# Optimization experiments

Measured on AMD Instinct MI355X. Metric: run time of the kernel, lower is better.

The kernel has to match this reference:

```python
import jax, jax.numpy as jnp
import numpy as np

FP8_MAX = 448.0  # torch.finfo(torch.float8_e4m3fn).max

def per_tensor_quantize(t):
    amax = jnp.max(jnp.abs(t))
    scale = FP8_MAX / jnp.maximum(amax, 1e-12)
    q = jnp.clip(t * scale, -FP8_MAX, FP8_MAX).astype(jnp.float8_e4m3fn)
    return q, (1.0 / scale).astype(jnp.float32)

def fp8_gemm(q, a_scale, w_q, w_scale, out_dtype):
    # emulate: linear(A.to(out)*a_scale, B.to(out)*b_scale)
    A = q.astype(out_dtype) * a_scale
    B = w_q.astype(out_dtype) * w_scale
    return A @ B.T

def setup_inputs() -> dict:
    key = jax.random.key(0)
    k1, k2, k3, k4 = jax.random.split(key, 4)
    tokens, hidden, ffn = 4096, 4096, 10752
    return {
        "x": jax.random.normal(k1, (tokens, hidden), jnp.float32),
        "expert_w1": jax.random.normal(k2, (ffn, hidden), jnp.float32) * 0.02,
        "expert_v1": jax.random.normal(k3, (ffn, hidden), jnp.float32) * 0.02,
        "expert_w2": jax.random.normal(k4, (ffn, hidden), jnp.float32) * 0.02,
    }

def reference(x, expert_w1, expert_v1, expert_w2):
    dt = x.dtype
    # weight quantization (as done in _quantize_weights per expert)
    w1_q, w1_s = per_tensor_quantize(expert_w1)
    v1_q, v1_s = per_tensor_quantize(expert_v1)
    w2_q, w2_s = per_tensor_quantize(expert_w2)
    # activation quantization + gate/up GEMMs
    qin, x_s = per_tensor_quantize(x)
    gate = fp8_gemm(qin, x_s, w1_q, w1_s, dt)          # [N, ffn]
    up = fp8_gemm(qin, x_s, v1_q, v1_s, dt)            # [N, ffn]
    inter = jax.nn.silu(gate) * up                      # fused GLU
    qmid, m_s = per_tensor_quantize(inter)
    # down proj uses expert_w2.t() -> B = [hidden, ffn]
    down = fp8_gemm(qmid, m_s, w2_q.T, w2_s, dt)        # [N, hidden]
    return down
```

## Files before the change

kernel.cpp:

```cpp
#include <hip/hip_runtime.h>
#include <cstdint>
#include <cstddef>

typedef float f32x4 __attribute__((ext_vector_type(4)));
typedef float f32x16 __attribute__((ext_vector_type(16)));
typedef int i32x4 __attribute__((ext_vector_type(4)));
typedef int i32x8 __attribute__((ext_vector_type(8)));
typedef unsigned char u8;

static __device__ __forceinline__ void gload_lds16(const void* g, void* l) {
  __builtin_amdgcn_global_load_lds(
      (__attribute__((address_space(1))) void*)(void*)g,
      (__attribute__((address_space(3))) void*)l,
      16, 0, 0);
}

#if defined(__has_builtin)
#if __has_builtin(__builtin_amdgcn_cvt_pk_fp8_f32)
#define HAVE_HW_FP8 1
#endif
#endif

__device__ __forceinline__ u8 f32_to_e4m3_sw(float x) {
  unsigned s = (__float_as_uint(x) >> 24) & 0x80;
  float ax = fabsf(x);
  if (!(ax > 0.0f)) return (u8)s;
  if (ax >= 448.0f) return (u8)(s | 0x7e);
  if (ax < 0.015625f) {
    int m = (int)rintf(ax * 512.0f);
    if (m >= 8) return (u8)(s | 0x08);
    return (u8)(s | m);
  }
  int e = ilogbf(ax);
  int m = (int)rintf(ldexpf(ax, 3 - e));
  if (m == 16) { ++e; m = 8; }
  return (u8)(s | ((e + 7) << 3) | (m - 8));
}

__device__ __forceinline__ unsigned cvt4_fp8(float a, float b, float c, float d) {
#ifdef HAVE_HW_FP8
  int lo = __builtin_amdgcn_cvt_pk_fp8_f32(a, b, 0, false);
  return (unsigned)__builtin_amdgcn_cvt_pk_fp8_f32(c, d, lo, true);
#else
  return (unsigned)f32_to_e4m3_sw(a) | ((unsigned)f32_to_e4m3_sw(b) << 8) |
         ((unsigned)f32_to_e4m3_sw(c) << 16) | ((unsigned)f32_to_e4m3_sw(d) << 24);
#endif
}

__global__ __launch_bounds__(256) void amax_kernel(const float* __restrict__ src, size_t n4,
                                                   unsigned* __restrict__ out) {
  float m = 0.0f;
  size_t stride = (size_t)gridDim.x * blockDim.x;
  const f32x4* p = (const f32x4*)src;
  for (size_t i = (size_t)blockIdx.x * blockDim.x + threadIdx.x; i < n4; i += stride) {
    f32x4 v = p[i];
    m = fmaxf(m, fmaxf(fmaxf(fabsf(v[0]), fabsf(v[1])), fmaxf(fabsf(v[2]), fabsf(v[3]))));
  }
#pragma unroll
  for (int off = 32; off > 0; off >>= 1) m = fmaxf(m, __shfl_down(m, off));
  __shared__ float red[4];
  int lane = threadIdx.x & 63, wid = threadIdx.x >> 6;
  if (lane == 0) red[wid] = m;
  __syncthreads();
  if (threadIdx.x == 0) {
    float v = fmaxf(fmaxf(red[0], red[1]), fmaxf(red[2], red[3]));
    atomicMax(out, __float_as_uint(v));
  }
}

__global__ __launch_bounds__(256) void quant_kernel(const float* __restrict__ src,
                                                    u8* __restrict__ dst,
                                                    const unsigned* __restrict__ amax_bits,
                                                    size_t n8) {
  float amax = __uint_as_float(*amax_bits);
  float scale = 448.0f / fmaxf(amax, 1e-12f);
  size_t stride = (size_t)gridDim.x * blockDim.x;
  const f32x4* p = (const f32x4*)src;
  uint2* q = (uint2*)dst;
  for (size_t i = (size_t)blockIdx.x * blockDim.x + threadIdx.x; i < n8; i += stride) {
    f32x4 a = p[2 * i], b = p[2 * i + 1];
    float a0 = fminf(fmaxf(a[0] * scale, -448.f), 448.f);
    float a1 = fminf(fmaxf(a[1] * scale, -448.f), 448.f);
    float a2 = fminf(fmaxf(a[2] * scale, -448.f), 448.f);
    float a3 = fminf(fmaxf(a[3] * scale, -448.f), 448.f);
    float b0 = fminf(fmaxf(b[0] * scale, -448.f), 448.f);
    float b1 = fminf(fmaxf(b[1] * scale, -448.f), 448.f);
    float b2 = fminf(fmaxf(b[2] * scale, -448.f), 448.f);
    float b3 = fminf(fmaxf(b[3] * scale, -448.f), 448.f);
    uint2 r;
    r.x = cvt4_fp8(a0, a1, a2, a3);
    r.y = cvt4_fp8(b0, b1, b2, b3);
    q[i] = r;
  }
}

__global__ __launch_bounds__(256) void quantT_kernel(const float* __restrict__ src,
                                                     u8* __restrict__ dst,
                                                     const unsigned* __restrict__ amax_bits,
                                                     int R, int C) {
  __shared__ float t[64][65];
  float amax = __uint_as_float(*amax_bits);
  float scale = 448.0f / fmaxf(amax, 1e-12f);
  int nbr = R >> 6;
  int br = (int)blockIdx.x % nbr, bc = (int)blockIdx.x / nbr;
  int r0 = br * 64, c0 = bc * 64;
  int tid = threadIdx.x;
  int lc = tid & 63, lr = tid >> 6;
#pragma unroll
  for (int i = 0; i < 16; ++i)
    t[lr + i * 4][lc] = src[(size_t)(r0 + lr + i * 4) * C + c0 + lc];
  __syncthreads();
  int qd = tid & 15, xbase = tid >> 4;
#pragma unroll
  for (int i = 0; i < 4; ++i) {
    int x = xbase + 16 * i;
    float v0 = fminf(fmaxf(t[4 * qd + 0][x] * scale, -448.f), 448.f);
    float v1 = fminf(fmaxf(t[4 * qd + 1][x] * scale, -448.f), 448.f);
    float v2 = fminf(fmaxf(t[4 * qd + 2][x] * scale, -448.f), 448.f);
    float v3 = fminf(fmaxf(t[4 * qd + 3][x] * scale, -448.f), 448.f);
    *(unsigned*)(dst + (size_t)(c0 + x) * R + r0 + 4 * qd) = cvt4_fp8(v0, v1, v2, v3);
  }
}

__device__ __forceinline__ int swz_key(int r) { return (r >> 2) & 3; }

__device__ __forceinline__ int swz_off32(int r, int h) {
  return r * 64 + ((((h << 1) ^ swz_key(r)) << 4));
}

__device__ __forceinline__ i32x8 ld_frag(const u8* base, int r, int h) {
  int o = swz_off32(r, h);
  i32x8 f;
  f.lo = *(const i32x4*)(base + o);
  f.hi = *(const i32x4*)(base + (o ^ 16));
  return f;
}

#define MFMA_MX(a, b, c) \
  __builtin_amdgcn_mfma_scale_f32_32x32x64_f8f6f4((a), (b), (c), 0, 0, 0, 0x7F7F7F7F, 0, 0x7F7F7F7F)

__global__ __launch_bounds__(512, 4) void gemm1_gateup(
    const u8* __restrict__ Aq, const u8* __restrict__ Wq, const u8* __restrict__ Vq,
    const unsigned* __restrict__ scal, float* __restrict__ inter,
    unsigned* __restrict__ amax_mid, int M, int N, int K) {
  __shared__ __align__(16) u8 lA[8192], lW[8192], lV[8192];
  __shared__ float red[8];
  int tid = threadIdx.x;
  int lane = tid & 63, wid = tid >> 6;
  int wm = wid >> 2, wn = wid & 3;

  int nbn = N >> 7;
  int nwg = (int)gridDim.x;
  int bid = (int)blockIdx.x;
  int cpx = nwg >> 3;
  int swz = (bid & 7) * cpx + (bid >> 3);
  int bm = swz / nbn, bn = swz - bm * nbn;

  int r0 = tid >> 2;
  int kblk = ((tid & 3) ^ swz_key(r0)) << 4;
  const u8* aS = Aq + (size_t)(bm * 128 + r0) * K + kblk;
  const u8* wS = Wq + (size_t)(bn * 128 + r0) * K + kblk;
  const u8* vS = Vq + (size_t)(bn * 128 + r0) * K + kblk;

  f32x16 g0 = (f32x16)(0.f), g1 = (f32x16)(0.f);
  f32x16 u0 = (f32x16)(0.f), u1 = (f32x16)(0.f);

  int rfrag = lane & 31;
  int h = lane >> 5;
  int arow = wm * 64 + rfrag;
  int wrow = wn * 32 + rfrag;

  for (int kt = 0; kt < K; kt += 64) {
    __syncthreads();
    gload_lds16(aS + kt, lA + tid * 16);
    gload_lds16(wS + kt, lW + tid * 16);
    gload_lds16(vS + kt, lV + tid * 16);
    __syncthreads();
    i32x8 a0 = ld_frag(lA, arow, h);
    i32x8 a1 = ld_frag(lA, arow + 32, h);
    i32x8 w0 = ld_frag(lW, wrow, h);
    i32x8 v0 = ld_frag(lV, wrow, h);
    g0 = MFMA_MX(a0, w0, g0);
    g1 = MFMA_MX(a1, w0, g1);
    u0 = MFMA_MX(a0, v0, u0);
    u1 = MFMA_MX(a1, v0, u1);
  }

  float ax = __uint_as_float(scal[0]);
  float aw = __uint_as_float(scal[1]);
  float av = __uint_as_float(scal[2]);
  float inv_x = 1.0f / (448.0f / fmaxf(ax, 1e-12f));
  float inv_w = 1.0f / (448.0f / fmaxf(aw, 1e-12f));
  float inv_v = 1.0f / (448.0f / fmaxf(av, 1e-12f));
  float sg = inv_x * inv_w, su = inv_x * inv_v;

  int rb = bm * 128 + wm * 64 + h * 4;
  int cb = bn * 128 + wn * 32 + rfrag;
  float lmax = 0.0f;
#pragma unroll
  for (int mi = 0; mi < 2; ++mi) {
    const f32x16& gg = mi ? g1 : g0;
    const f32x16& uu = mi ? u1 : u0;
#pragma unroll
    for (int q = 0; q < 16; ++q) {
      int rr = rb + mi * 32 + (q & 3) + 8 * (q >> 2);
      float gv = gg[q] * sg;
      float uv = uu[q] * su;
      float iv = gv / (1.0f + expf(-gv)) * uv;
      inter[(size_t)rr * N + cb] = iv;
      lmax = fmaxf(lmax, fabsf(iv));
    }
  }
#pragma unroll
  for (int off = 32; off > 0; off >>= 1) lmax = fmaxf(lmax, __shfl_down(lmax, off));
  if (lane == 0) red[wid] = lmax;
  __syncthreads();
  if (tid == 0) {
    float v = red[0];
#pragma unroll
    for (int i = 1; i < 8; ++i) v = fmaxf(v, red[i]);
    atomicMax(amax_mid, __float_as_uint(v));
  }
}

__global__ __launch_bounds__(512, 4) void gemm2_down(
    const u8* __restrict__ Aq, const u8* __restrict__ Bq,
    const unsigned* __restrict__ amax_a, const unsigned* __restrict__ amax_b,
    float* __restrict__ out, int M, int N, int K) {
  __shared__ __align__(16) u8 lA[8192], lB[16384];
  int tid = threadIdx.x;
  int lane = tid & 63, wid = tid >> 6;
  int wm = wid >> 2, wn = wid & 3;

  int nbn = N >> 8;
  int nwg = (int)gridDim.x;
  int bid = (int)blockIdx.x;
  int cpx = nwg >> 3;
  int swz = (bid & 7) * cpx + (bid >> 3);
  int bm = swz / nbn, bn = swz - bm * nbn;

  int r0 = tid >> 2;
  int kblk = ((tid & 3) ^ swz_key(r0)) << 4;
  const u8* aS = Aq + (size_t)(bm * 128 + r0) * K + kblk;
  const u8* bS = Bq + (size_t)(bn * 256 + r0) * K + kblk;
  size_t rK = (size_t)128 * K;

  f32x16 c00 = (f32x16)(0.f), c01 = (f32x16)(0.f);
  f32x16 c10 = (f32x16)(0.f), c11 = (f32x16)(0.f);

  int rfrag = lane & 31;
  int h = lane >> 5;
  int arow = wm * 64 + rfrag;
  int brow = wn * 64 + rfrag;

  for (int kt = 0; kt < K; kt += 64) {
    __syncthreads();
    gload_lds16(aS + kt, lA + tid * 16);
    gload_lds16(bS + kt, lB + tid * 16);
    gload_lds16(bS + kt + rK, lB + 8192 + tid * 16);
    __syncthreads();
    i32x8 a0 = ld_frag(lA, arow, h);
    i32x8 a1 = ld_frag(lA, arow + 32, h);
    i32x8 b0 = ld_frag(lB, brow, h);
    i32x8 b1 = ld_frag(lB, brow + 32, h);
    c00 = MFMA_MX(a0, b0, c00);
    c01 = MFMA_MX(a0, b1, c01);
    c10 = MFMA_MX(a1, b0, c10);
    c11 = MFMA_MX(a1, b1, c11);
  }

  float sa = 1.0f / (448.0f / fmaxf(__uint_as_float(*amax_a), 1e-12f));
  float sb = 1.0f / (448.0f / fmaxf(__uint_as_float(*amax_b), 1e-12f));
  float sc = sa * sb;

  int rb = bm * 128 + wm * 64 + h * 4;
  int cb = bn * 256 + wn * 64 + rfrag;
#pragma unroll
  for (int mi = 0; mi < 2; ++mi)
#pragma unroll
    for (int ni = 0; ni < 2; ++ni) {
      const f32x16& cc = mi ? (ni ? c11 : c10) : (ni ? c01 : c00);
#pragma unroll
      for (int q = 0; q < 16; ++q) {
        int rr = rb + mi * 32 + (q & 3) + 8 * (q >> 2);
        out[(size_t)rr * N + (cb + ni * 32)] = cc[q] * sc;
      }
    }
}

extern "C" void kernel_launch(void* const* d_in, const int* in_sizes, int n_in,
                              void* d_out, int out_size, void* d_ws, size_t ws_size,
                              hipStream_t stream) {
  const float* x  = (const float*)d_in[0];
  const float* w1 = (const float*)d_in[1];
  const float* v1 = (const float*)d_in[2];
  const float* w2 = (const float*)d_in[3];
  const int M = 4096, H = 4096, F = 10752;

  u8* ws = (u8*)d_ws;
  unsigned* scal = (unsigned*)ws;
  u8* xq   = ws + 256;
  u8* w1q  = xq   + (size_t)M * H;
  u8* v1q  = w1q  + (size_t)F * H;
  u8* w2qT = v1q  + (size_t)F * H;
  u8* midq = w2qT + (size_t)F * H;
  float* inter = (float*)(midq + (size_t)M * F);

  hipMemsetAsync(scal, 0, 256, stream);
  amax_kernel<<<2048, 256, 0, stream>>>(x,  (size_t)M * H / 4, scal + 0);
  amax_kernel<<<2048, 256, 0, stream>>>(w1, (size_t)F * H / 4, scal + 1);
  amax_kernel<<<2048, 256, 0, stream>>>(v1, (size_t)F * H / 4, scal + 2);
  amax_kernel<<<2048, 256, 0, stream>>>(w2, (size_t)F * H / 4, scal + 3);

  quant_kernel<<<2048, 256, 0, stream>>>(x,  xq,  scal + 0, (size_t)M * H / 8);
  quant_kernel<<<2048, 256, 0, stream>>>(w1, w1q, scal + 1, (size_t)F * H / 8);
  quant_kernel<<<2048, 256, 0, stream>>>(v1, v1q, scal + 2, (size_t)F * H / 8);
  quantT_kernel<<<(F / 64) * (H / 64), 256, 0, stream>>>(w2, w2qT, scal + 3, F, H);

  gemm1_gateup<<<(M / 128) * (F / 128), 512, 0, stream>>>(xq, w1q, v1q, scal, inter,
                                                          scal + 4, M, F, H);
  quant_kernel<<<2048, 256, 0, stream>>>(inter, midq, scal + 4, (size_t)M * F / 8);
  gemm2_down<<<(M / 128) * (H / 256), 512, 0, stream>>>(midq, w2qT, scal + 4, scal + 3,
                                                        (float*)d_out, M, H, F);
}
```

Measured before the change: 1.018 ms.

## Triple-buffer LDS with async prefetch and 4-wave tiles in both FP8 GEMMs

Both GEMM kernels move from 8-wave blocks with a load/sync/compute loop to 4-wave blocks that each compute a 64x64 sub-tile. K-tiles go into a 3-stage LDS ring, with prefetches issued two tiles ahead, explicit vmcnt waits, barriers and MFMA priority bumps, so global-to-LDS loads overlap the MFMA work. gemm2 shrinks its N tile from 256 to 128, which doubles its grid. In exchange, LDS use per block rises and each wave holds more accumulator registers, which may reduce occupancy.

```diff
diff --git a/kernel.cpp b/kernel.cpp
--- a/kernel.cpp
+++ b/kernel.cpp
@@ -139,15 +139,15 @@
 #define MFMA_MX(a, b, c) \
   __builtin_amdgcn_mfma_scale_f32_32x32x64_f8f6f4((a), (b), (c), 0, 0, 0, 0x7F7F7F7F, 0, 0x7F7F7F7F)
 
-__global__ __launch_bounds__(512, 4) void gemm1_gateup(
+__global__ __launch_bounds__(256, 2) void gemm1_gateup(
     const u8* __restrict__ Aq, const u8* __restrict__ Wq, const u8* __restrict__ Vq,
     const unsigned* __restrict__ scal, float* __restrict__ inter,
     unsigned* __restrict__ amax_mid, int M, int N, int K) {
-  __shared__ __align__(16) u8 lA[8192], lW[8192], lV[8192];
-  __shared__ float red[8];
+  __shared__ __align__(16) u8 lA[3][8192], lW[3][8192], lV[3][8192];
+  __shared__ float red[4];
   int tid = threadIdx.x;
   int lane = tid & 63, wid = tid >> 6;
-  int wm = wid >> 2, wn = wid & 3;
+  int wm = wid >> 1, wn = wid & 1;
 
   int nbn = N >> 7;
   int nwg = (int)gridDim.x;
@@ -161,29 +161,74 @@
   const u8* aS = Aq + (size_t)(bm * 128 + r0) * K + kblk;
   const u8* wS = Wq + (size_t)(bn * 128 + r0) * K + kblk;
   const u8* vS = Vq + (size_t)(bn * 128 + r0) * K + kblk;
-
-  f32x16 g0 = (f32x16)(0.f), g1 = (f32x16)(0.f);
-  f32x16 u0 = (f32x16)(0.f), u1 = (f32x16)(0.f);
+  size_t rK = (size_t)64 * K;
+
+  f32x16 g00 = (f32x16)(0.f), g01 = (f32x16)(0.f), g10 = (f32x16)(0.f), g11 = (f32x16)(0.f);
+  f32x16 u00 = (f32x16)(0.f), u01 = (f32x16)(0.f), u10 = (f32x16)(0.f), u11 = (f32x16)(0.f);
 
   int rfrag = lane & 31;
   int h = lane >> 5;
   int arow = wm * 64 + rfrag;
-  int wrow = wn * 32 + rfrag;
-
-  for (int kt = 0; kt < K; kt += 64) {
-    __syncthreads();
-    gload_lds16(aS + kt, lA + tid * 16);
-    gload_lds16(wS + kt, lW + tid * 16);
-    gload_lds16(vS + kt, lV + tid * 16);
-    __syncthreads();
-    i32x8 a0 = ld_frag(lA, arow, h);
-    i32x8 a1 = ld_frag(lA, arow + 32, h);
-    i32x8 w0 = ld_frag(lW, wrow, h);
-    i32x8 v0 = ld_frag(lV, wrow, h);
-    g0 = MFMA_MX(a0, w0, g0);
-    g1 = MFMA_MX(a1, w0, g1);
-    u0 = MFMA_MX(a0, v0, u0);
-    u1 = MFMA_MX(a1, v0, u1);
+  int brow = wn * 64 + rfrag;
+
+  int NT = K >> 6;
+  {
+    gload_lds16(aS + 0, lA[0] + tid * 16);
+    gload_lds16(aS + 0 + rK, lA[0] + 4096 + tid * 16);
+    gload_lds16(wS + 0, lW[0] + tid * 16);
+    gload_lds16(wS + 0 + rK, lW[0] + 4096 + tid * 16);
+    gload_lds16(vS + 0, lV[0] + tid * 16);
+    gload_lds16(vS + 0 + rK, lV[0] + 4096 + tid * 16);
+    gload_lds16(aS + 64, lA[1] + tid * 16);
+    gload_lds16(aS + 64 + rK, lA[1] + 4096 + tid * 16);
+    gload_lds16(wS + 64, lW[1] + tid * 16);
+    gload_lds16(wS + 64 + rK, lW[1] + 4096 + tid * 16);
+    gload_lds16(vS + 64, lV[1] + tid * 16);
+    gload_lds16(vS + 64 + rK, lV[1] + 4096 + tid * 16);
+  }
+
+  for (int t = 0; t < NT; ++t) {
+    int cur = t % 3;
+    int nx = cur + 2; if (nx >= 3) nx -= 3;
+    int kt2 = (t + 2) * 64;
+    bool do_stage = (t + 2) < NT;
+    if (t + 1 < NT) {
+      asm volatile("s_waitcnt vmcnt(6)" ::: "memory");
+    } else {
+      asm volatile("s_waitcnt vmcnt(0)" ::: "memory");
+    }
+    __builtin_amdgcn_s_barrier();
+    i32x8 a0 = ld_frag(lA[cur], arow, h);
+    i32x8 a1 = ld_frag(lA[cur], arow + 32, h);
+    i32x8 w0 = ld_frag(lW[cur], brow, h);
+    i32x8 w1 = ld_frag(lW[cur], brow + 32, h);
+    if (do_stage) {
+      gload_lds16(aS + kt2, lA[nx] + tid * 16);
+      gload_lds16(aS + kt2 + rK, lA[nx] + 4096 + tid * 16);
+      gload_lds16(wS + kt2, lW[nx] + tid * 16);
+    }
+    __builtin_amdgcn_s_barrier();
+    __builtin_amdgcn_s_setprio(1);
+    g00 = MFMA_MX(a0, w0, g00);
+    g10 = MFMA_MX(a1, w0, g10);
+    g01 = MFMA_MX(a0, w1, g01);
+    g11 = MFMA_MX(a1, w1, g11);
+    __builtin_amdgcn_s_setprio(0);
+    __builtin_amdgcn_s_barrier();
+    i32x8 v0 = ld_frag(lV[cur], brow, h);
+    i32x8 v1 = ld_frag(lV[cur], brow + 32, h);
+    if (do_stage) {
+      gload_lds16(wS + kt2 + rK, lW[nx] + 4096 + tid * 16);
+      gload_lds16(vS + kt2, lV[nx] + tid * 16);
+      gload_lds16(vS + kt2 + rK, lV[nx] + 4096 + tid * 16);
+    }
+    __builtin_amdgcn_s_barrier();
+    __builtin_amdgcn_s_setprio(1);
+    u00 = MFMA_MX(a0, v0, u00);
+    u10 = MFMA_MX(a1, v0, u10);
+    u01 = MFMA_MX(a0, v1, u01);
+    u11 = MFMA_MX(a1, v1, u11);
+    __builtin_amdgcn_s_setprio(0);
   }
 
   float ax = __uint_as_float(scal[0]);
@@ -195,44 +240,42 @@
   float sg = inv_x * inv_w, su = inv_x * inv_v;
 
   int rb = bm * 128 + wm * 64 + h * 4;
-  int cb = bn * 128 + wn * 32 + rfrag;
+  int cb = bn * 128 + wn * 64 + rfrag;
   float lmax = 0.0f;
 #pragma unroll
-  for (int mi = 0; mi < 2; ++mi) {
-    const f32x16& gg = mi ? g1 : g0;
-    const f32x16& uu = mi ? u1 : u0;
-#pragma unroll
-    for (int q = 0; q < 16; ++q) {
-      int rr = rb + mi * 32 + (q & 3) + 8 * (q >> 2);
-      float gv = gg[q] * sg;
-      float uv = uu[q] * su;
-      float iv = gv / (1.0f + expf(-gv)) * uv;
-      inter[(size_t)rr * N + cb] = iv;
-      lmax = fmaxf(lmax, fabsf(iv));
-    }
-  }
+  for (int mi = 0; mi < 2; ++mi)
+#pragma unroll
+    for (int ni = 0; ni < 2; ++ni) {
+      const f32x16& gg = mi ? (ni ? g11 : g10) : (ni ? g01 : g00);
+      const f32x16& uu = mi ? (ni ? u11 : u10) : (ni ? u01 : u00);
+#pragma unroll
+      for (int q = 0; q < 16; ++q) {
+        int rr = rb + mi * 32 + (q & 3) + 8 * (q >> 2);
+        float gv = gg[q] * sg;
+        float uv = uu[q] * su;
+        float iv = gv / (1.0f + expf(-gv)) * uv;
+        inter[(size_t)rr * N + (cb + ni * 32)] = iv;
+        lmax = fmaxf(lmax, fabsf(iv));
+      }
+    }
 #pragma unroll
   for (int off = 32; off > 0; off >>= 1) lmax = fmaxf(lmax, __shfl_down(lmax, off));
   if (lane == 0) red[wid] = lmax;
   __syncthreads();
-  if (tid == 0) {
-    float v = red[0];
-#pragma unroll
-    for (int i = 1; i < 8; ++i) v = fmaxf(v, red[i]);
-    atomicMax(amax_mid, __float_as_uint(v));
-  }
-}
-
-__global__ __launch_bounds__(512, 4) void gemm2_down(
+  if (tid == 0)
+    atomicMax(amax_mid, __float_as_uint(fmaxf(fmaxf(red[0], red[1]), fmaxf(red[2], red[3]))));
+}
+
+__global__ __launch_bounds__(256, 2) void gemm2_down(
     const u8* __restrict__ Aq, const u8* __restrict__ Bq,
     const unsigned* __restrict__ amax_a, const unsigned* __restrict__ amax_b,
     float* __restrict__ out, int M, int N, int K) {
-  __shared__ __align__(16) u8 lA[8192], lB[16384];
+  __shared__ __align__(16) u8 lA[3][8192], lB[3][8192];
   int tid = threadIdx.x;
   int lane = tid & 63, wid = tid >> 6;
-  int wm = wid >> 2, wn = wid & 3;
-
-  int nbn = N >> 8;
+  int wm = wid >> 1, wn = wid & 1;
+
+  int nbn = N >> 7;
   int nwg = (int)gridDim.x;
   int bid = (int)blockIdx.x;
   int cpx = nwg >> 3;
@@ -242,8 +285,8 @@
   int r0 = tid >> 2;
   int kblk = ((tid & 3) ^ swz_key(r0)) << 4;
   const u8* aS = Aq + (size_t)(bm * 128 + r0) * K + kblk;
-  const u8* bS = Bq + (size_t)(bn * 256 + r0) * K + kblk;
-  size_t rK = (size_t)128 * K;
+  const u8* bS = Bq + (size_t)(bn * 128 + r0) * K + kblk;
+  size_t rK = (size_t)64 * K;
 
   f32x16 c00 = (f32x16)(0.f), c01 = (f32x16)(0.f);
   f32x16 c10 = (f32x16)(0.f), c11 = (f32x16)(0.f);
@@ -253,20 +296,52 @@
   int arow = wm * 64 + rfrag;
   int brow = wn * 64 + rfrag;
 
-  for (int kt = 0; kt < K; kt += 64) {
-    __syncthreads();
-    gload_lds16(aS + kt, lA + tid * 16);
-    gload_lds16(bS + kt, lB + tid * 16);
-    gload_lds16(bS + kt + rK, lB + 8192 + tid * 16);
-    __syncthreads();
-    i32x8 a0 = ld_frag(lA, arow, h);
-    i32x8 a1 = ld_frag(lA, arow + 32, h);
-    i32x8 b0 = ld_frag(lB, brow, h);
-    i32x8 b1 = ld_frag(lB, brow + 32, h);
+  int NT = K >> 6;
+  {
+    gload_lds16(aS + 0, lA[0] + tid * 16);
+    gload_lds16(aS + 0 + rK, lA[0] + 4096 + tid * 16);
+    gload_lds16(bS + 0, lB[0] + tid * 16);
+    gload_lds16(bS + 0 + rK, lB[0] + 4096 + tid * 16);
+    gload_lds16(aS + 64, lA[1] + tid * 16);
+    gload_lds16(aS + 64 + rK, lA[1] + 4096 + tid * 16);
+    gload_lds16(bS + 64, lB[1] + tid * 16);
+    gload_lds16(bS + 64 + rK, lB[1] + 4096 + tid * 16);
+  }
+
+  for (int t = 0; t < NT; ++t) {
+    int cur = t % 3;
+    int nx = cur + 2; if (nx >= 3) nx -= 3;
+    int kt2 = (t + 2) * 64;
+    bool do_stage = (t + 2) < NT;
+    if (t + 1 < NT) {
+      asm volatile("s_waitcnt vmcnt(4)" ::: "memory");
+    } else {
+      asm volatile("s_waitcnt vmcnt(0)" ::: "memory");
+    }
+    __builtin_amdgcn_s_barrier();
+    i32x8 a0 = ld_frag(lA[cur], arow, h);
+    i32x8 a1 = ld_frag(lA[cur], arow + 32, h);
+    i32x8 b0 = ld_frag(lB[cur], brow, h);
+    if (do_stage) {
+      gload_lds16(aS + kt2, lA[nx] + tid * 16);
+      gload_lds16(aS + kt2 + rK, lA[nx] + 4096 + tid * 16);
+    }
+    __builtin_amdgcn_s_barrier();
+    __builtin_amdgcn_s_setprio(1);
     c00 = MFMA_MX(a0, b0, c00);
+    c10 = MFMA_MX(a1, b0, c10);
+    __builtin_amdgcn_s_setprio(0);
+    __builtin_amdgcn_s_barrier();
+    i32x8 b1 = ld_frag(lB[cur], brow + 32, h);
+    if (do_stage) {
+      gload_lds16(bS + kt2, lB[nx] + tid * 16);
+      gload_lds16(bS + kt2 + rK, lB[nx] + 4096 + tid * 16);
+    }
+    __builtin_amdgcn_s_barrier();
+    __builtin_amdgcn_s_setprio(1);
     c01 = MFMA_MX(a0, b1, c01);
-    c10 = MFMA_MX(a1, b0, c10);
     c11 = MFMA_MX(a1, b1, c11);
+    __builtin_amdgcn_s_setprio(0);
   }
 
   float sa = 1.0f / (448.0f / fmaxf(__uint_as_float(*amax_a), 1e-12f));
@@ -274,7 +349,7 @@
   float sc = sa * sb;
 
   int rb = bm * 128 + wm * 64 + h * 4;
-  int cb = bn * 256 + wn * 64 + rfrag;
+  int cb = bn * 128 + wn * 64 + rfrag;
 #pragma unroll
   for (int mi = 0; mi < 2; ++mi)
 #pragma unroll
@@ -317,9 +392,9 @@
   quant_kernel<<<2048, 256, 0, stream>>>(v1, v1q, scal + 2, (size_t)F * H / 8);
   quantT_kernel<<<(F / 64) * (H / 64), 256, 0, stream>>>(w2, w2qT, scal + 3, F, H);
 
-  gemm1_gateup<<<(M / 128) * (F / 128), 512, 0, stream>>>(xq, w1q, v1q, scal, inter,
+  gemm1_gateup<<<(M / 128) * (F / 128), 256, 0, stream>>>(xq, w1q, v1q, scal, inter,
                                                           scal + 4, M, F, H);
   quant_kernel<<<2048, 256, 0, stream>>>(inter, midq, scal + 4, (size_t)M * F / 8);
-  gemm2_down<<<(M / 128) * (H / 256), 512, 0, stream>>>(midq, w2qT, scal + 4, scal + 3,
+  gemm2_down<<<(M / 128) * (H / 128), 256, 0, stream>>>(midq, w2qT, scal + 4, scal + 3,
                                                         (float*)d_out, M, H, F);
 }
```

Result: slower. 1.077 ms (+5.8%).
